# Optimization experiments

Hardware: AMD Instinct MI355X
Metric: run time of the kernel (lower is better)

Reference implementation:

```python
import jax, jax.numpy as jnp
import numpy as np

B, L, D_MODEL, D_FF, N_EXPERTS, TOP_K = 32, 256, 512, 2048, 8, 2
EPS = 1e-9


def setup_inputs() -> dict:
    key = jax.random.key(0)
    ks = jax.random.split(key, 7)
    scale1 = 1.0 / np.sqrt(D_MODEL)
    scale2 = 1.0 / np.sqrt(D_FF)
    return {
        "cycle_curve_data": jax.random.normal(ks[0], (B, L, D_MODEL), jnp.float32),
        "logits": jax.random.normal(ks[1], (B, N_EXPERTS), jnp.float32),
        "moe_masks": jax.random.randint(ks[2], (B, N_EXPERTS), 0, 2, jnp.int32),
        "W1": jax.random.normal(ks[3], (N_EXPERTS, D_MODEL, D_FF), jnp.float32) * scale1,
        "b1": jax.random.normal(ks[4], (N_EXPERTS, D_FF), jnp.float32) * scale1,
        "W2": jax.random.normal(ks[5], (N_EXPERTS, D_FF, D_MODEL), jnp.float32) * scale2,
        "b2": jax.random.normal(ks[6], (N_EXPERTS, D_MODEL), jnp.float32) * scale2,
    }


def _gates(logits, moe_masks):
    # softmax over experts, zero out unavailable experts, keep top-k, renormalize
    mask = (moe_masks == 1).astype(logits.dtype)               # [B, E]
    p = jax.nn.softmax(logits, axis=1) * mask                  # [B, E]
    _, idx = jax.lax.top_k(p, TOP_K)                           # [B, K]
    topk_mask = jnp.zeros_like(p).at[jnp.arange(p.shape[0])[:, None], idx].set(1.0)
    p = p * topk_mask
    return p / (jnp.sum(p, axis=1, keepdims=True) + EPS)       # [B, E]


def reference(cycle_curve_data, logits, moe_masks, W1, b1, W2, b2):
    gates = _gates(logits, moe_masks)                          # [B, E]
    x = cycle_curve_data                                       # [B, L, D]
    # dense equivalent of per-expert gather -> MLP -> gate-weighted scatter-combine
    h = jnp.einsum("bld,edf->eblf", x, W1) + b1[:, None, None, :]   # [E,B,L,F]
    h = jax.nn.gelu(h, approximate=False)
    out = jnp.einsum("be,eblf,efd->bld", gates, h, W2)
    out = out + jnp.einsum("be,ed->bd", gates, b2)[:, None, :]      # [B,L,D]
    return out
```

## Files before the change

kernel.cpp:

```cpp
#include <hip/hip_runtime.h>

#define B_SZ 32
#define L_SZ 256
#define D_SZ 512
#define F_SZ 2048
#define E_SZ 8
#define P_SZ 64
#define BK2  32

typedef __attribute__((ext_vector_type(8)))  short bf16x8;
typedef __attribute__((ext_vector_type(16))) float f32x16;

__device__ __forceinline__ unsigned short f2bf(float f) {
  unsigned int u = __builtin_bit_cast(unsigned int, f);
  u += 0x7fffu + ((u >> 16) & 1u);
  return (unsigned short)(u >> 16);
}

__device__ __forceinline__ void async16(const void* g, void* l) {
  __builtin_amdgcn_global_load_lds(
      (const __attribute__((address_space(1))) unsigned int*)g,
      (__attribute__((address_space(3))) unsigned int*)l, 16, 0, 0);
}

__device__ __forceinline__ float gelu_f(float x) {
  float a = fabsf(x) * 0.70710678118654752f;
  float t = __builtin_amdgcn_rcpf(1.0f + 0.3275911f * a);
  float y = t * (0.254829592f +
            t * (-0.284496736f +
            t * (1.421413741f +
            t * (-1.453152027f +
            t * 1.061405429f))));
  float e = __expf(-a * a);
  float erf_abs = 1.0f - y * e;
  float erf_v = (x < 0.f) ? -erf_abs : erf_abs;
  return 0.5f * x * (1.0f + erf_v);
}

__device__ __forceinline__ void transpose_tile(
    const float* __restrict__ ip, unsigned short* __restrict__ op,
    int R, int C, int r0, int c0, float* tile, int tid) {
  int tx = tid & 63, ty = tid >> 6;
#pragma unroll
  for (int i = 0; i < 16; ++i) {
    int r = i * 4 + ty;
    tile[r * 65 + tx] = ip[(size_t)(r0 + r) * C + c0 + tx];
  }
  __syncthreads();
#pragma unroll
  for (int uu = 0; uu < 4; ++uu) {
    int u = uu * 256 + tid;
    int cc = u >> 4, q = u & 15;
    ushort4 o;
    o.x = f2bf(tile[(q * 4 + 0) * 65 + cc]);
    o.y = f2bf(tile[(q * 4 + 1) * 65 + cc]);
    o.z = f2bf(tile[(q * 4 + 2) * 65 + cc]);
    o.w = f2bf(tile[(q * 4 + 3) * 65 + cc]);
    *(ushort4*)(op + (size_t)(c0 + cc) * R + r0 + q * 4) = o;
  }
}

#define PREP_CONV_BLKS 4096
#define PREP_TR_BLKS   2048
#define PREP_TOTAL     (1 + PREP_CONV_BLKS + PREP_TR_BLKS)

__global__ __launch_bounds__(256) void prep_kernel(
    const float* __restrict__ logits, const int* __restrict__ masks,
    const float* __restrict__ x,
    const float* __restrict__ W1,
    int* __restrict__ sel_e, float* __restrict__ sel_g,
    unsigned short* __restrict__ xb,
    unsigned short* __restrict__ w1t) {
  __shared__ float tile[64 * 65];
  int blk = blockIdx.x;
  int tid = threadIdx.x;

  if (blk == 0) {
    int b = tid;
    if (b >= B_SZ) return;
    float lg[E_SZ], p[E_SZ];
    float mx = -1e30f;
    for (int e = 0; e < E_SZ; ++e) { lg[e] = logits[b * E_SZ + e]; mx = fmaxf(mx, lg[e]); }
    float s = 0.f;
    for (int e = 0; e < E_SZ; ++e) { p[e] = expf(lg[e] - mx); s += p[e]; }
    for (int e = 0; e < E_SZ; ++e) p[e] = (masks[b * E_SZ + e] == 1) ? (p[e] / s) : 0.f;
    int i0 = 0, i1 = 1; float v0 = -1.f, v1 = -1.f;
    for (int e = 0; e < E_SZ; ++e) {
      float v = p[e];
      if (v > v0)      { v1 = v0; i1 = i0; v0 = v; i0 = e; }
      else if (v > v1) { v1 = v;  i1 = e; }
    }
    float den = v0 + v1 + 1e-9f;
    sel_e[2 * b] = i0;  sel_e[2 * b + 1] = i1;
    sel_g[2 * b] = v0 / den;
    sel_g[2 * b + 1] = v1 / den;
    return;
  }
  blk -= 1;

  if (blk < PREP_CONV_BLKS) {
    int i = blk * 256 + tid;
    float4 v = ((const float4*)x)[i];
    ushort4 o;
    o.x = f2bf(v.x); o.y = f2bf(v.y); o.z = f2bf(v.z); o.w = f2bf(v.w);
    ((ushort4*)xb)[i] = o;
    return;
  }
  blk -= PREP_CONV_BLKS;

  int z = blk >> 8;
  int rem = blk & 255;
  int tr = rem >> 5, tc = rem & 31;
  transpose_tile(W1 + (size_t)z * D_SZ * F_SZ, w1t + (size_t)z * D_SZ * F_SZ,
                 D_SZ, F_SZ, tr * 64, tc * 64, tile, tid);
}

__global__ __launch_bounds__(256, 4) void moe_gemm1(
    const unsigned short* __restrict__ Xb,
    const unsigned short* __restrict__ W1t,
    const float* __restrict__ b1,
    const int* __restrict__ sel_e,
    unsigned short* __restrict__ H,
    const float* __restrict__ W2,
    unsigned short* __restrict__ w2t) {
  __shared__ __align__(16) char smem[32768];
  int tid = threadIdx.x;
  int lin = blockIdx.x;

  if (lin >= 2048) {
    int blk = lin - 2048;
    int z = blk >> 8;
    int rem = blk & 255;
    int tr = rem >> 3, tc = rem & 7;
    transpose_tile(W2 + (size_t)z * F_SZ * D_SZ, w2t + (size_t)z * F_SZ * D_SZ,
                   F_SZ, D_SZ, tr * 64, tc * 64, (float*)smem, tid);
    return;
  }

  unsigned short* As = (unsigned short*)smem;
  unsigned short* Bs = (unsigned short*)(smem + 16384);

  int f  = lin & 15;
  int l0 = ((lin >> 4) & 1) * 128;
  int p  = lin >> 5;
  int f0 = f * 128;
  int b  = p >> 1;
  int e  = sel_e[p];

  int lane = tid & 63;
  int w = tid >> 6, wm = w & 1, wn = w >> 1;
  int m32 = lane & 31, kh = lane >> 5;
  int sw = (m32 >> 1) & 3;

  const unsigned short* Abase = Xb  + ((size_t)b * L_SZ + l0) * D_SZ;
  const unsigned short* Bbase = W1t + ((size_t)e * F_SZ + f0) * D_SZ;

  int seg0 = w * 128 + lane;
  int row0 = seg0 >> 2, ks0 = ((seg0 & 3) ^ ((row0 >> 1) & 3)) * 8;
  int seg1 = seg0 + 64;
  int row1 = seg1 >> 2, ks1 = ((seg1 & 3) ^ ((row1 >> 1) & 3)) * 8;

  f32x16 acc[2][2] = {};

  for (int k0 = 0; k0 < D_SZ; k0 += 2 * BK2) {
#pragma unroll
    for (int h = 0; h < 2; ++h) {
      int kk = k0 + h * BK2;
      async16(Abase + (size_t)row0 * D_SZ + kk + ks0, &As[(h * 512 + seg0) * 8]);
      async16(Abase + (size_t)row1 * D_SZ + kk + ks1, &As[(h * 512 + seg1) * 8]);
      async16(Bbase + (size_t)row0 * D_SZ + kk + ks0, &Bs[(h * 512 + seg0) * 8]);
      async16(Bbase + (size_t)row1 * D_SZ + kk + ks1, &Bs[(h * 512 + seg1) * 8]);
    }
    __syncthreads();
#pragma unroll
    for (int h = 0; h < 2; ++h)
#pragma unroll
      for (int s = 0; s < 2; ++s) {
        int ko = ((((s << 1) | kh) ^ sw) << 3) + h * 4096;
        bf16x8 a0  = *(const bf16x8*)&As[(wm * 64 +      m32) * BK2 + ko];
        bf16x8 a1  = *(const bf16x8*)&As[(wm * 64 + 32 + m32) * BK2 + ko];
        bf16x8 b0  = *(const bf16x8*)&Bs[(wn * 64 +      m32) * BK2 + ko];
        bf16x8 b1f = *(const bf16x8*)&Bs[(wn * 64 + 32 + m32) * BK2 + ko];
        acc[0][0] = __builtin_amdgcn_mfma_f32_32x32x16_bf16(a0, b0,  acc[0][0], 0, 0, 0);
        acc[0][1] = __builtin_amdgcn_mfma_f32_32x32x16_bf16(a0, b1f, acc[0][1], 0, 0, 0);
        acc[1][0] = __builtin_amdgcn_mfma_f32_32x32x16_bf16(a1, b0,  acc[1][0], 0, 0, 0);
        acc[1][1] = __builtin_amdgcn_mfma_f32_32x32x16_bf16(a1, b1f, acc[1][1], 0, 0, 0);
      }
    __syncthreads();
  }

  float b1v[2];
#pragma unroll
  for (int tj = 0; tj < 2; ++tj)
    b1v[tj] = b1[e * F_SZ + f0 + wn * 64 + tj * 32 + m32];

  unsigned short* Hp = H + ((size_t)p * L_SZ + l0) * F_SZ + f0;
#pragma unroll
  for (int ti = 0; ti < 2; ++ti)
#pragma unroll
    for (int tj = 0; tj < 2; ++tj) {
      int col = wn * 64 + tj * 32 + m32;
#pragma unroll
      for (int r = 0; r < 16; ++r) {
        int row = wm * 64 + ti * 32 + (r & 3) + 8 * (r >> 2) + 4 * kh;
        Hp[(size_t)row * F_SZ + col] = f2bf(gelu_f(acc[ti][tj][r] + b1v[tj]));
      }
    }
}

__global__ __launch_bounds__(256, 4) void moe_gemm2(
    const unsigned short* __restrict__ H,
    const unsigned short* __restrict__ W2t,
    const float* __restrict__ b2,
    const int* __restrict__ sel_e,
    const float* __restrict__ sel_g,
    float* __restrict__ part,
    float* __restrict__ Out) {
  __shared__ __align__(16) unsigned short As[2][128 * BK2];
  __shared__ __align__(16) unsigned short Bs[2][128 * BK2];

  int lin = blockIdx.x;
  int q   = lin & 7;
  int d   = (lin >> 3) & 3;
  int g8  = lin >> 5;
  int gg  = g8 * 8 + q;
  int p   = gg >> 1;
  int l0  = (gg & 1) * 128;
  int d0  = d * 128;
  int b   = p >> 1;
  int e   = sel_e[p];
  float g = sel_g[p];

  int tid = threadIdx.x;
  int lane = tid & 63;
  int w = tid >> 6, wm = w & 1, wn = w >> 1;
  int m32 = lane & 31, kh = lane >> 5;
  int sw = (m32 >> 1) & 3;

  const unsigned short* Abase = H   + ((size_t)p * L_SZ + l0) * F_SZ;
  const unsigned short* Bbase = W2t + ((size_t)e * D_SZ + d0) * F_SZ;

  int seg0 = w * 128 + lane;
  int row0 = seg0 >> 2, ks0 = ((seg0 & 3) ^ ((row0 >> 1) & 3)) * 8;
  int seg1 = seg0 + 64;
  int row1 = seg1 >> 2, ks1 = ((seg1 & 3) ^ ((row1 >> 1) & 3)) * 8;

  f32x16 acc[2][2] = {};

  for (int k0 = 0; k0 < F_SZ; k0 += 2 * BK2) {
#pragma unroll
    for (int h = 0; h < 2; ++h) {
      int kk = k0 + h * BK2;
      async16(Abase + (size_t)row0 * F_SZ + kk + ks0, &As[h][seg0 * 8]);
      async16(Abase + (size_t)row1 * F_SZ + kk + ks1, &As[h][seg1 * 8]);
      async16(Bbase + (size_t)row0 * F_SZ + kk + ks0, &Bs[h][seg0 * 8]);
      async16(Bbase + (size_t)row1 * F_SZ + kk + ks1, &Bs[h][seg1 * 8]);
    }
    __syncthreads();
#pragma unroll
    for (int h = 0; h < 2; ++h)
#pragma unroll
      for (int s = 0; s < 2; ++s) {
        int ko = (((s << 1) | kh) ^ sw) << 3;
        bf16x8 a0  = *(const bf16x8*)&As[h][(wm * 64 +      m32) * BK2 + ko];
        bf16x8 a1  = *(const bf16x8*)&As[h][(wm * 64 + 32 + m32) * BK2 + ko];
        bf16x8 b0  = *(const bf16x8*)&Bs[h][(wn * 64 +      m32) * BK2 + ko];
        bf16x8 b1f = *(const bf16x8*)&Bs[h][(wn * 64 + 32 + m32) * BK2 + ko];
        acc[0][0] = __builtin_amdgcn_mfma_f32_32x32x16_bf16(a0, b0,  acc[0][0], 0, 0, 0);
        acc[0][1] = __builtin_amdgcn_mfma_f32_32x32x16_bf16(a0, b1f, acc[0][1], 0, 0, 0);
        acc[1][0] = __builtin_amdgcn_mfma_f32_32x32x16_bf16(a1, b0,  acc[1][0], 0, 0, 0);
        acc[1][1] = __builtin_amdgcn_mfma_f32_32x32x16_bf16(a1, b1f, acc[1][1], 0, 0, 0);
      }
    __syncthreads();
  }

  float bias[2] = {0.f, 0.f};
  if (p & 1) {
    int e0 = sel_e[2 * b], e1 = sel_e[2 * b + 1];
    float g0 = sel_g[2 * b], g1 = sel_g[2 * b + 1];
#pragma unroll
    for (int tj = 0; tj < 2; ++tj) {
      int dd = d0 + wn * 64 + tj * 32 + m32;
      bias[tj] = g0 * b2[e0 * D_SZ + dd] + g1 * b2[e1 * D_SZ + dd];
    }
  }
  float* dst = (p & 1) ? Out : part;
  float* Op = dst + ((size_t)b * L_SZ + l0) * D_SZ + d0;
#pragma unroll
  for (int ti = 0; ti < 2; ++ti)
#pragma unroll
    for (int tj = 0; tj < 2; ++tj) {
      int col = wn * 64 + tj * 32 + m32;
#pragma unroll
      for (int r = 0; r < 16; ++r) {
        int row = wm * 64 + ti * 32 + (r & 3) + 8 * (r >> 2) + 4 * kh;
        Op[(size_t)row * D_SZ + col] = g * acc[ti][tj][r] + bias[tj];
      }
    }
}

__global__ __launch_bounds__(256) void combine_kernel(
    const float* __restrict__ part, float* __restrict__ Out) {
  int i = blockIdx.x * 256 + threadIdx.x;
  float4 pv = ((const float4*)part)[i];
  float4 o  = ((float4*)Out)[i];
  o.x += pv.x; o.y += pv.y; o.z += pv.z; o.w += pv.w;
  ((float4*)Out)[i] = o;
}

extern "C" void kernel_launch(void* const* d_in, const int* in_sizes, int n_in,
                              void* d_out, int out_size, void* d_ws, size_t ws_size,
                              hipStream_t stream) {
  const float* x      = (const float*)d_in[0];
  const float* logits = (const float*)d_in[1];
  const int*   masks  = (const int*)d_in[2];
  const float* W1     = (const float*)d_in[3];
  const float* b1     = (const float*)d_in[4];
  const float* W2     = (const float*)d_in[5];
  const float* b2     = (const float*)d_in[6];
  float* out = (float*)d_out;

  char* ws = (char*)d_ws;
  int*   sel_e = (int*)ws;
  float* sel_g = (float*)(ws + 256);
  unsigned short* xb  = (unsigned short*)(ws + 1024);
  unsigned short* w1t = xb  + (size_t)B_SZ * L_SZ * D_SZ;
  unsigned short* w2t = w1t + (size_t)E_SZ * F_SZ * D_SZ;
  unsigned short* Hbuf = w2t + (size_t)E_SZ * D_SZ * F_SZ;
  float* part = (float*)(ws + 1024);

  prep_kernel<<<PREP_TOTAL, 256, 0, stream>>>(logits, masks, x, W1,
                                              sel_e, sel_g, xb, w1t);
  moe_gemm1<<<4096, 256, 0, stream>>>(xb, w1t, b1, sel_e, Hbuf, W2, w2t);
  moe_gemm2<<<512, 256, 0, stream>>>(Hbuf, w2t, b2, sel_e, sel_g, part, out);
  combine_kernel<<<(B_SZ * L_SZ * D_SZ / 4) / 256, 256, 0, stream>>>(part, out);
}
```

Baseline: 230.3 us.

## Double-buffer LDS tiles to overlap async loads with MFMA in both GEMMs

Both expert GEMM kernels switch from load-two-tiles-then-compute-two-tiles to a ping-pong pipeline. The next K tile is issued with async global-to-LDS loads while the MFMAs consume the current buffer, with one barrier per step instead of two per pair of tiles. The aim is to hide global memory latency behind matrix math. The trade-off is that the async loads may not be explicitly waited on before the barrier, so correctness depends on how the compiler inserts vmcnt waits at __syncthreads; the loop also has a prologue and epilogue.

```diff
diff --git a/kernel.cpp b/kernel.cpp
--- a/kernel.cpp
+++ b/kernel.cpp
@@ -160,34 +160,44 @@
   int seg1 = seg0 + 64;
   int row1 = seg1 >> 2, ks1 = ((seg1 & 3) ^ ((row1 >> 1) & 3)) * 8;
 
+  const size_t aoff0 = (size_t)row0 * D_SZ + ks0;
+  const size_t aoff1 = (size_t)row1 * D_SZ + ks1;
+
   f32x16 acc[2][2] = {};
 
-  for (int k0 = 0; k0 < D_SZ; k0 += 2 * BK2) {
-#pragma unroll
-    for (int h = 0; h < 2; ++h) {
-      int kk = k0 + h * BK2;
-      async16(Abase + (size_t)row0 * D_SZ + kk + ks0, &As[(h * 512 + seg0) * 8]);
-      async16(Abase + (size_t)row1 * D_SZ + kk + ks1, &As[(h * 512 + seg1) * 8]);
-      async16(Bbase + (size_t)row0 * D_SZ + kk + ks0, &Bs[(h * 512 + seg0) * 8]);
-      async16(Bbase + (size_t)row1 * D_SZ + kk + ks1, &Bs[(h * 512 + seg1) * 8]);
-    }
+#define G1_COMPUTE(CB)                                                       \
+  _Pragma("unroll")                                                          \
+  for (int s = 0; s < 2; ++s) {                                              \
+    int ko = ((((s << 1) | kh) ^ sw) << 3) + (CB) * 4096;                    \
+    bf16x8 a0  = *(const bf16x8*)&As[(wm * 64 +      m32) * BK2 + ko];       \
+    bf16x8 a1  = *(const bf16x8*)&As[(wm * 64 + 32 + m32) * BK2 + ko];       \
+    bf16x8 b0  = *(const bf16x8*)&Bs[(wn * 64 +      m32) * BK2 + ko];       \
+    bf16x8 b1f = *(const bf16x8*)&Bs[(wn * 64 + 32 + m32) * BK2 + ko];       \
+    acc[0][0] = __builtin_amdgcn_mfma_f32_32x32x16_bf16(a0, b0,  acc[0][0], 0, 0, 0); \
+    acc[0][1] = __builtin_amdgcn_mfma_f32_32x32x16_bf16(a0, b1f, acc[0][1], 0, 0, 0); \
+    acc[1][0] = __builtin_amdgcn_mfma_f32_32x32x16_bf16(a1, b0,  acc[1][0], 0, 0, 0); \
+    acc[1][1] = __builtin_amdgcn_mfma_f32_32x32x16_bf16(a1, b1f, acc[1][1], 0, 0, 0); \
+  }
+
+  async16(Abase + aoff0, &As[seg0 * 8]);
+  async16(Abase + aoff1, &As[seg1 * 8]);
+  async16(Bbase + aoff0, &Bs[seg0 * 8]);
+  async16(Bbase + aoff1, &Bs[seg1 * 8]);
+  __syncthreads();
+
+#pragma unroll 2
+  for (int t = 0; t < 15; ++t) {
+    int cb = t & 1, nb = cb ^ 1;
+    int kk = (t + 1) * BK2;
+    async16(Abase + aoff0 + kk, &As[(nb * 512 + seg0) * 8]);
+    async16(Abase + aoff1 + kk, &As[(nb * 512 + seg1) * 8]);
+    async16(Bbase + aoff0 + kk, &Bs[(nb * 512 + seg0) * 8]);
+    async16(Bbase + aoff1 + kk, &Bs[(nb * 512 + seg1) * 8]);
+    G1_COMPUTE(cb)
     __syncthreads();
-#pragma unroll
-    for (int h = 0; h < 2; ++h)
-#pragma unroll
-      for (int s = 0; s < 2; ++s) {
-        int ko = ((((s << 1) | kh) ^ sw) << 3) + h * 4096;
-        bf16x8 a0  = *(const bf16x8*)&As[(wm * 64 +      m32) * BK2 + ko];
-        bf16x8 a1  = *(const bf16x8*)&As[(wm * 64 + 32 + m32) * BK2 + ko];
-        bf16x8 b0  = *(const bf16x8*)&Bs[(wn * 64 +      m32) * BK2 + ko];
-        bf16x8 b1f = *(const bf16x8*)&Bs[(wn * 64 + 32 + m32) * BK2 + ko];
-        acc[0][0] = __builtin_amdgcn_mfma_f32_32x32x16_bf16(a0, b0,  acc[0][0], 0, 0, 0);
-        acc[0][1] = __builtin_amdgcn_mfma_f32_32x32x16_bf16(a0, b1f, acc[0][1], 0, 0, 0);
-        acc[1][0] = __builtin_amdgcn_mfma_f32_32x32x16_bf16(a1, b0,  acc[1][0], 0, 0, 0);
-        acc[1][1] = __builtin_amdgcn_mfma_f32_32x32x16_bf16(a1, b1f, acc[1][1], 0, 0, 0);
-      }
-    __syncthreads();
-  }
+  }
+  G1_COMPUTE(1)
+#undef G1_COMPUTE
 
   float b1v[2];
 #pragma unroll
@@ -216,8 +226,8 @@
     const float* __restrict__ sel_g,
     float* __restrict__ part,
     float* __restrict__ Out) {
-  __shared__ __align__(16) unsigned short As[2][128 * BK2];
-  __shared__ __align__(16) unsigned short Bs[2][128 * BK2];
+  __shared__ __align__(16) unsigned short As[2][512 * 8];
+  __shared__ __align__(16) unsigned short Bs[2][512 * 8];
 
   int lin = blockIdx.x;
   int q   = lin & 7;
@@ -245,34 +255,44 @@
   int seg1 = seg0 + 64;
   int row1 = seg1 >> 2, ks1 = ((seg1 & 3) ^ ((row1 >> 1) & 3)) * 8;
 
+  const size_t aoff0 = (size_t)row0 * F_SZ + ks0;
+  const size_t aoff1 = (size_t)row1 * F_SZ + ks1;
+
   f32x16 acc[2][2] = {};
 
-  for (int k0 = 0; k0 < F_SZ; k0 += 2 * BK2) {
-#pragma unroll
-    for (int h = 0; h < 2; ++h) {
-      int kk = k0 + h * BK2;
-      async16(Abase + (size_t)row0 * F_SZ + kk + ks0, &As[h][seg0 * 8]);
-      async16(Abase + (size_t)row1 * F_SZ + kk + ks1, &As[h][seg1 * 8]);
-      async16(Bbase + (size_t)row0 * F_SZ + kk + ks0, &Bs[h][seg0 * 8]);
-      async16(Bbase + (size_t)row1 * F_SZ + kk + ks1, &Bs[h][seg1 * 8]);
-    }
+#define G2_COMPUTE(CB)                                                       \
+  _Pragma("unroll")                                                          \
+  for (int s = 0; s < 2; ++s) {                                              \
+    int ko = ((((s << 1) | kh) ^ sw) << 3);                                  \
+    bf16x8 a0  = *(const bf16x8*)&As[CB][(wm * 64 +      m32) * BK2 + ko];   \
+    bf16x8 a1  = *(const bf16x8*)&As[CB][(wm * 64 + 32 + m32) * BK2 + ko];   \
+    bf16x8 b0  = *(const bf16x8*)&Bs[CB][(wn * 64 +      m32) * BK2 + ko];   \
+    bf16x8 b1f = *(const bf16x8*)&Bs[CB][(wn * 64 + 32 + m32) * BK2 + ko];   \
+    acc[0][0] = __builtin_amdgcn_mfma_f32_32x32x16_bf16(a0, b0,  acc[0][0], 0, 0, 0); \
+    acc[0][1] = __builtin_amdgcn_mfma_f32_32x32x16_bf16(a0, b1f, acc[0][1], 0, 0, 0); \
+    acc[1][0] = __builtin_amdgcn_mfma_f32_32x32x16_bf16(a1, b0,  acc[1][0], 0, 0, 0); \
+    acc[1][1] = __builtin_amdgcn_mfma_f32_32x32x16_bf16(a1, b1f, acc[1][1], 0, 0, 0); \
+  }
+
+  async16(Abase + aoff0, &As[0][seg0 * 8]);
+  async16(Abase + aoff1, &As[0][seg1 * 8]);
+  async16(Bbase + aoff0, &Bs[0][seg0 * 8]);
+  async16(Bbase + aoff1, &Bs[0][seg1 * 8]);
+  __syncthreads();
+
+#pragma unroll 2
+  for (int t = 0; t < 63; ++t) {
+    int cb = t & 1, nb = cb ^ 1;
+    int kk = (t + 1) * BK2;
+    async16(Abase + aoff0 + kk, &As[nb][seg0 * 8]);
+    async16(Abase + aoff1 + kk, &As[nb][seg1 * 8]);
+    async16(Bbase + aoff0 + kk, &Bs[nb][seg0 * 8]);
+    async16(Bbase + aoff1 + kk, &Bs[nb][seg1 * 8]);
+    G2_COMPUTE(cb)
     __syncthreads();
-#pragma unroll
-    for (int h = 0; h < 2; ++h)
-#pragma unroll
-      for (int s = 0; s < 2; ++s) {
-        int ko = (((s << 1) | kh) ^ sw) << 3;
-        bf16x8 a0  = *(const bf16x8*)&As[h][(wm * 64 +      m32) * BK2 + ko];
-        bf16x8 a1  = *(const bf16x8*)&As[h][(wm * 64 + 32 + m32) * BK2 + ko];
-        bf16x8 b0  = *(const bf16x8*)&Bs[h][(wn * 64 +      m32) * BK2 + ko];
-        bf16x8 b1f = *(const bf16x8*)&Bs[h][(wn * 64 + 32 + m32) * BK2 + ko];
-        acc[0][0] = __builtin_amdgcn_mfma_f32_32x32x16_bf16(a0, b0,  acc[0][0], 0, 0, 0);
-        acc[0][1] = __builtin_amdgcn_mfma_f32_32x32x16_bf16(a0, b1f, acc[0][1], 0, 0, 0);
-        acc[1][0] = __builtin_amdgcn_mfma_f32_32x32x16_bf16(a1, b0,  acc[1][0], 0, 0, 0);
-        acc[1][1] = __builtin_amdgcn_mfma_f32_32x32x16_bf16(a1, b1f, acc[1][1], 0, 0, 0);
-      }
-    __syncthreads();
-  }
+  }
+  G2_COMPUTE(1)
+#undef G2_COMPUTE
 
   float bias[2] = {0.f, 0.f};
   if (p & 1) {
```

Result: slower. 242.1 us (+5.1%).
